# Optimization experiments

Hardware: AMD Instinct MI355X
Metric: run time of the kernel (lower is better)

The kernel has to match this reference:

```python
import jax, jax.numpy as jnp
import numpy as np

N, E, F, G, C, L = 20000, 320000, 75, 64, 10, 5
EPS = 1e-5


def setup_inputs():
    key = jax.random.key(0)
    ks = jax.random.split(key, 16)
    x = jax.random.normal(ks[0], (N, 6), jnp.float32)
    edge_index = jax.random.randint(ks[1], (2, E), 0, N, dtype=jnp.int32)
    batch = jnp.sort(jax.random.randint(ks[2], (N,), 0, G, dtype=jnp.int32))
    gcn_w = jax.random.normal(ks[3], (6, F), jnp.float32) / np.sqrt(6.0)
    gcn_b = jnp.zeros((F,), jnp.float32)
    pre_w = jax.random.normal(ks[4], (L, 2 * F, F), jnp.float32) / np.sqrt(2.0 * F)
    pre_b = jnp.zeros((L, F), jnp.float32)
    post_w = jax.random.normal(ks[5], (L, 13 * F, F), jnp.float32) / np.sqrt(13.0 * F)
    post_b = jnp.zeros((L, F), jnp.float32)
    lin_w = jax.random.normal(ks[6], (L, F, F), jnp.float32) / np.sqrt(1.0 * F)
    lin_b = jnp.zeros((L, F), jnp.float32)
    bn_g = jnp.ones((L, F), jnp.float32)
    bn_b = jnp.zeros((L, F), jnp.float32)
    w1 = jax.random.normal(ks[7], (F, 50), jnp.float32) / np.sqrt(1.0 * F)
    b1 = jnp.zeros((50,), jnp.float32)
    w2 = jax.random.normal(ks[8], (50, 25), jnp.float32) / np.sqrt(50.0)
    b2 = jnp.zeros((25,), jnp.float32)
    w3 = jax.random.normal(ks[9], (25, C), jnp.float32) / np.sqrt(25.0)
    b3 = jnp.zeros((C,), jnp.float32)
    return dict(x=x, edge_index=edge_index, batch=batch, gcn_w=gcn_w, gcn_b=gcn_b,
                pre_w=pre_w, pre_b=pre_b, post_w=post_w, post_b=post_b,
                lin_w=lin_w, lin_b=lin_b, bn_g=bn_g, bn_b=bn_b,
                w1=w1, b1=b1, w2=w2, b2=b2, w3=w3, b3=b3)


def reference(x, edge_index, batch, gcn_w, gcn_b, pre_w, pre_b, post_w, post_b,
              lin_w, lin_b, bn_g, bn_b, w1, b1, w2, b2, w3, b3):
    row, col = edge_index[0], edge_index[1]  # messages flow row (j) -> col (i)
    ones_e = jnp.ones((E,), jnp.float32)

    # ---- GCNConv(6, 75) with self-loops and symmetric normalization ----
    xw = x @ gcn_w                                   # [N, F]
    deg = jax.ops.segment_sum(ones_e, col, N) + 1.0  # in-degree + self-loop
    dinv = 1.0 / jnp.sqrt(deg)
    norm_e = (dinv[row] * dinv[col])[:, None]        # [E, 1]
    h = jax.ops.segment_sum(norm_e * xw[row], col, N) + (dinv * dinv)[:, None] * xw + gcn_b

    # ---- degree-based scalers (shared by all PNA layers) ----
    cnt = jax.ops.segment_sum(ones_e, col, N)        # in-degree per node
    avg_log = jnp.mean(jnp.log(cnt + 1.0))           # avg_deg['log'] from this graph's degree histogram
    d = jnp.maximum(cnt, 1.0)
    amp = (jnp.log(d + 1.0) / avg_log)[:, None]      # amplification
    att = (avg_log / jnp.log(d + 1.0))[:, None]      # attenuation
    cnt_c = jnp.maximum(cnt, 1.0)[:, None]
    has_nb = (cnt > 0)[:, None]

    for l in range(L):
        # pre-MLP on [x_i, x_j] per edge
        m = jnp.concatenate([h[col], h[row]], axis=-1) @ pre_w[l] + pre_b[l]  # [E, F]
        s = jax.ops.segment_sum(m, col, N)
        mean = s / cnt_c
        mean_sq = jax.ops.segment_sum(m * m, col, N) / cnt_c
        std = jnp.sqrt(jax.nn.relu(mean_sq - mean * mean) + EPS)
        mn = jnp.where(has_nb, jax.ops.segment_min(m, col, N), 0.0)
        mx = jnp.where(has_nb, jax.ops.segment_max(m, col, N), 0.0)
        agg = jnp.concatenate([mean, mn, mx, std], axis=-1)          # [N, 4F]
        scaled = jnp.concatenate([agg, agg * amp, agg * att], -1)    # [N, 12F]
        o = jnp.concatenate([h, scaled], axis=-1) @ post_w[l] + post_b[l]  # post-MLP
        o = o @ lin_w[l] + lin_b[l]                                  # final lin
        mu = o.mean(axis=0)
        var = o.var(axis=0)
        o = (o - mu) / jnp.sqrt(var + EPS) * bn_g[l] + bn_b[l]       # BatchNorm (batch stats)
        h = jax.nn.relu(o)

    # ---- global_add_pool + MLP (dropout = identity in eval) ----
    g = jax.ops.segment_sum(h, batch, G)
    g = jax.nn.relu(g @ w1 + b1)
    g = jax.nn.relu(g @ w2 + b2)
    return g @ w3 + b3  # [G, C]
```

## Files before the change

### kernel.cpp

```cpp
#include <hip/hip_runtime.h>
#include <hip/hip_bf16.h>

#define NN 20000
#define EE 320000
#define FF 75
#define GG 64
#define LL 5
#define EPS 1e-5f

#define KUV 96
#define NUV 160
#define KPOST 384
#define KLIN 96

typedef short bf16x8 __attribute__((ext_vector_type(8)));
typedef float f32x4 __attribute__((ext_vector_type(4)));

__device__ inline void gAtomicAdd(float* p, float v) { unsafeAtomicAdd(p, v); }

__device__ inline ushort f2bs(float x) {
    __hip_bfloat16 b = __float2bfloat16(x);
    return *(ushort*)&b;
}

__device__ inline float bs2f(ushort u) {
    unsigned int x = ((unsigned int)u) << 16;
    return __uint_as_float(x);
}


__global__ void count_kernel(const int* __restrict__ col, int* __restrict__ cnt, int E) {
    int e = blockIdx.x * blockDim.x + threadIdx.x;
    if (e < E) atomicAdd(&cnt[col[e]], 1);
}

__global__ void dinv_partial_kernel(const int* __restrict__ cnt, float* __restrict__ dinv,
                                    float* __restrict__ scal, int* __restrict__ bsum, int N) {
    __shared__ float red[256];
    __shared__ int redi[256];
    int tid = threadIdx.x;
    int i = blockIdx.x * 256 + tid;
    float lg = 0.f;
    int cv = 0;
    if (i < N) {
        cv = cnt[i];
        float c = (float)cv;
        dinv[i] = 1.f / sqrtf(c + 1.f);
        lg = logf(c + 1.f);
    }
    red[tid] = lg;
    redi[tid] = cv;
    __syncthreads();
    for (int s = 128; s > 0; s >>= 1) {
        if (tid < s) { red[tid] += red[tid + s]; redi[tid] += redi[tid + s]; }
        __syncthreads();
    }
    if (tid == 0) {
        gAtomicAdd(&scal[0], red[0]);
        bsum[blockIdx.x] = redi[0];
    }
}

__global__ void scanb_kernel(const int* __restrict__ bsum, int* __restrict__ bbase,
                             int* __restrict__ offs, int NB) {
    __shared__ int sh[128];
    int tid = threadIdx.x;
    int v = (tid < NB) ? bsum[tid] : 0;
    sh[tid] = v;
    __syncthreads();
    for (int d = 1; d < 128; d <<= 1) {
        int t = (tid >= d) ? sh[tid - d] : 0;
        __syncthreads();
        sh[tid] += t;
        __syncthreads();
    }
    if (tid < NB) bbase[tid] = sh[tid] - v;
    if (tid == 0) offs[NN] = EE;
}

__global__ void offs_kernel(const int* __restrict__ cnt, const int* __restrict__ bbase,
                            int* __restrict__ offs, int* __restrict__ cursor, int N) {
    __shared__ int sh[256];
    int tid = threadIdx.x;
    int i = blockIdx.x * 256 + tid;
    int v = (i < N) ? cnt[i] : 0;
    sh[tid] = v;
    __syncthreads();
    for (int d = 1; d < 256; d <<= 1) {
        int t = (tid >= d) ? sh[tid - d] : 0;
        __syncthreads();
        sh[tid] += t;
        __syncthreads();
    }
    int excl = sh[tid] - v + bbase[blockIdx.x];
    if (i < N) { offs[i] = excl; cursor[i] = excl; }
}

__global__ void fill_xs_kernel(const int* __restrict__ row, const int* __restrict__ col,
                               int* __restrict__ cursor, int* __restrict__ csr,
                               const float* __restrict__ x, const float* __restrict__ gw,
                               const float* __restrict__ dinv, ushort* __restrict__ xs) {
    int idx = blockIdx.x * 256 + threadIdx.x;
    if (idx < EE) {
        int c = col[idx];
        int pos = atomicAdd(&cursor[c], 1);
        csr[pos] = row[idx];
    } else if (idx < EE + NN * 80) {
        int j = idx - EE;
        int n = j / 80, t = j % 80;
        float v = 0.f;
        if (t < FF) {
            float acc = 0.f;
#pragma unroll
            for (int k = 0; k < 6; k++) acc += x[n * 6 + k] * gw[k * FF + t];
            v = dinv[n] * acc;
        }
        xs[j] = f2bs(v);
    }
}

__global__ __launch_bounds__(64) void gcn_kernel(
    const ushort* __restrict__ xs, const float* __restrict__ dinv,
    const int* __restrict__ offs, const int* __restrict__ csr,
    const float* __restrict__ gcn_b, const int* __restrict__ cnt,
    const float* __restrict__ scal, float* __restrict__ o2,
    float* __restrict__ amp, float* __restrict__ att, int N) {
    int i = blockIdx.x;
    int lane = threadIdx.x;
    int s0 = offs[i], s1 = offs[i + 1];
    if (lane < 40) {
        float a0 = 0.f, a1 = 0.f;
        int k = s0;
        for (; k + 3 < s1; k += 4) {
            int r0 = csr[k], r1 = csr[k + 1], r2 = csr[k + 2], r3 = csr[k + 3];
            ushort2 v0 = *(const ushort2*)(xs + (size_t)r0 * 80 + 2 * lane);
            ushort2 v1 = *(const ushort2*)(xs + (size_t)r1 * 80 + 2 * lane);
            ushort2 v2 = *(const ushort2*)(xs + (size_t)r2 * 80 + 2 * lane);
            ushort2 v3 = *(const ushort2*)(xs + (size_t)r3 * 80 + 2 * lane);
            a0 += (bs2f(v0.x) + bs2f(v1.x)) + (bs2f(v2.x) + bs2f(v3.x));
            a1 += (bs2f(v0.y) + bs2f(v1.y)) + (bs2f(v2.y) + bs2f(v3.y));
        }
        for (; k < s1; k++) {
            int r0 = csr[k];
            ushort2 v0 = *(const ushort2*)(xs + (size_t)r0 * 80 + 2 * lane);
            a0 += bs2f(v0.x);
            a1 += bs2f(v0.y);
        }
        ushort2 vs = *(const ushort2*)(xs + (size_t)i * 80 + 2 * lane);
        a0 += bs2f(vs.x);
        a1 += bs2f(vs.y);
        float di = dinv[i];
        int t0 = 2 * lane, t1 = 2 * lane + 1;
        if (t0 < FF) o2[(size_t)i * 80 + t0] = di * a0 + gcn_b[t0];
        if (t1 < FF) o2[(size_t)i * 80 + t1] = di * a1 + gcn_b[t1];
    } else if (lane == 63) {
        float al = scal[0] / (float)N;
        float d = fmaxf((float)cnt[i], 1.f);
        float lg = logf(d + 1.f);
        amp[i] = lg / al;
        att[i] = al / lg;
    }
}


#define S_UV (LL * NUV * KUV)
#define S_POST (LL * 240 * KPOST)
#define S_LIN (LL * 80 * KLIN)

__global__ void prep_bt_kernel(const float* __restrict__ pre_w, const float* __restrict__ pre_b,
                               const float* __restrict__ post_w, const float* __restrict__ lin_w,
                               ushort* __restrict__ BTuv, ushort* __restrict__ BTpost,
                               ushort* __restrict__ BTlin) {
    int idx = blockIdx.x * 256 + threadIdx.x;
    if (idx < S_UV) {
        int l = idx / (NUV * KUV);
        int r = idx % (NUV * KUV);
        int c = r / KUV, k = r % KUV;
        float v = 0.f;
        if (k < FF) {
            if (c < FF) v = pre_w[((size_t)l * 150 + k) * FF + c];
            else if (c >= 80 && c < 80 + FF) v = pre_w[((size_t)l * 150 + FF + k) * FF + (c - 80)];
        } else if (k == FF && c < FF) {
            v = pre_b[l * FF + c];
        }
        BTuv[idx] = f2bs(v);
    } else if (idx < S_UV + S_POST) {
        int j = idx - S_UV;
        int l = j / (240 * KPOST);
        int r = j % (240 * KPOST);
        int c = r / KPOST, k = r % KPOST;
        float v = 0.f;
        if (k < FF) {
            if (c < FF) v = post_w[((size_t)l * 975 + k) * FF + c];
        } else if (k < 375) {
            if (c < FF) v = post_w[((size_t)l * 975 + k) * FF + c];
            else if (c >= 80 && c < 80 + FF) v = post_w[((size_t)l * 975 + k + 300) * FF + (c - 80)];
            else if (c >= 160 && c < 160 + FF) v = post_w[((size_t)l * 975 + k + 600) * FF + (c - 160)];
        }
        BTpost[j] = f2bs(v);
    } else if (idx < S_UV + S_POST + S_LIN) {
        int j = idx - S_UV - S_POST;
        int l = j / (80 * KLIN);
        int r = j % (80 * KLIN);
        int c = r / KLIN, k = r % KLIN;
        float v = (c < FF && k < FF) ? lin_w[((size_t)l * FF + k) * FF + c] : 0.f;
        BTlin[j] = f2bs(v);
    }
}


__global__ __launch_bounds__(64) void uv_bn_kernel(
    const float* __restrict__ o2, const float* __restrict__ slots,
    const float* __restrict__ bg, const float* __restrict__ bb, int apply_bn,
    const ushort* __restrict__ BT, float* __restrict__ U, ushort* __restrict__ Vb,
    ushort* __restrict__ hagg) {
    __shared__ float ssL[160];
    int lane = threadIdx.x;
    int col16 = lane & 15, quad = lane >> 4;
    int n = blockIdx.x * 16 + col16;
    const float* orow = o2 + (size_t)n * 80;
    const ushort* bbase = BT + (size_t)col16 * KUV + quad * 8;

    if (apply_bn) {
        for (int c = lane; c < 80; c += 64) {
            if (c < FF) {
                float su = 0.f, sq = 0.f;
#pragma unroll 8
                for (int s = 0; s < 32; s++) {
                    su += slots[s * 160 + c];
                    sq += slots[s * 160 + 80 + c];
                }
                float mu = su * (1.f / (float)NN);
                float var = sq * (1.f / (float)NN) - mu * mu;
                float sc = bg[c] * rsqrtf(var + EPS);
                ssL[c] = sc;
                ssL[80 + c] = bb[c] - mu * sc;
            } else {
                ssL[c] = 0.f;
                ssL[80 + c] = 0.f;
            }
        }
        __syncthreads();
    }

    f32x4 acc[10];
#pragma unroll
    for (int i = 0; i < 10; i++) acc[i] = (f32x4){0.f, 0.f, 0.f, 0.f};

#pragma unroll
    for (int kt = 0; kt < 3; kt++) {
        int kb = kt * 32 + quad * 8;
        bf16x8 af;
        if (kb < 80) {
            float4 v0 = *(const float4*)(orow + kb);
            float4 v1 = *(const float4*)(orow + kb + 4);
            float vv[8] = {v0.x, v0.y, v0.z, v0.w, v1.x, v1.y, v1.z, v1.w};
#pragma unroll
            for (int j = 0; j < 8; j++) {
                int k = kb + j;
                float v = vv[j];
                if (apply_bn) v = fmaxf(v * ssL[k] + ssL[80 + k], 0.f);
                ushort b = (k < FF) ? f2bs(v) : (k == FF ? (ushort)0x3F80 : (ushort)0);
                af[j] = (short)b;
            }
            if (kb < FF) {
                *(bf16x8*)(hagg + (size_t)n * KPOST + kb) = af;
            }
        } else {
            af = (bf16x8){0, 0, 0, 0, 0, 0, 0, 0};
        }
#pragma unroll
        for (int nt = 0; nt < 10; nt++) {
            bf16x8 bfr = *(const bf16x8*)(bbase + nt * (16 * KUV) + kt * 32);
            acc[nt] = __builtin_amdgcn_mfma_f32_16x16x32_bf16(af, bfr, acc[nt], 0, 0, 0);
        }
    }
    int n0 = blockIdx.x * 16;
#pragma unroll
    for (int nt = 0; nt < 10; nt++) {
        int col = nt * 16 + col16;
#pragma unroll
        for (int r = 0; r < 4; r++) {
            int nn = n0 + quad * 4 + r;
            if (col < FF) U[(size_t)nn * 80 + col] = acc[nt][r];
            else if (col >= 80 && col < 80 + FF) Vb[(size_t)nn * 80 + (col - 80)] = f2bs(acc[nt][r]);
        }
    }
}


__global__ __launch_bounds__(64) void post_lin_kernel(
    const ushort* __restrict__ A, const ushort* __restrict__ BT,
    const ushort* __restrict__ BL, const float* __restrict__ amp,
    const float* __restrict__ att, float* __restrict__ o2,
    float* __restrict__ slots) {
    __shared__ __align__(16) ushort olds[16 * 104];
    int lane = threadIdx.x;
    int col16 = lane & 15, quad = lane >> 4, kseg = quad * 8;
    int n0 = blockIdx.x * 16;
    const ushort* arow = A + (size_t)(n0 + col16) * KPOST + kseg;
    const ushort* bbase = BT + (size_t)col16 * KPOST + kseg;

    f32x4 acc[15];
#pragma unroll
    for (int i = 0; i < 15; i++) acc[i] = (f32x4){0.f, 0.f, 0.f, 0.f};

#pragma unroll 4
    for (int kt = 0; kt < 12; kt++) {
        bf16x8 af = *(const bf16x8*)(arow + kt * 32);
#pragma unroll
        for (int nt = 0; nt < 15; nt++) {
            bf16x8 bfr = *(const bf16x8*)(bbase + (size_t)nt * (16 * KPOST) + kt * 32);
            acc[nt] = __builtin_amdgcn_mfma_f32_16x16x32_bf16(af, bfr, acc[nt], 0, 0, 0);
        }
    }
    float ampv[4], attv[4];
#pragma unroll
    for (int r = 0; r < 4; r++) {
        int n = n0 + quad * 4 + r;
        ampv[r] = amp[n];
        attv[r] = att[n];
    }
#pragma unroll
    for (int g = 0; g < 5; g++) {
        int col = g * 16 + col16;
#pragma unroll
        for (int r = 0; r < 4; r++) {
            float ov = acc[g][r] + ampv[r] * acc[g + 5][r] + attv[r] * acc[g + 10][r];
            olds[(quad * 4 + r) * 104 + col] = (col < FF) ? f2bs(ov) : (ushort)0;
        }
    }
    *(ushort4*)(olds + (lane >> 2) * 104 + 80 + (lane & 3) * 4) = (ushort4){0, 0, 0, 0};
    __syncthreads();

    f32x4 acc2[5];
#pragma unroll
    for (int i = 0; i < 5; i++) acc2[i] = (f32x4){0.f, 0.f, 0.f, 0.f};
    const ushort* blbase = BL + (size_t)col16 * KLIN + kseg;
#pragma unroll
    for (int kt = 0; kt < 3; kt++) {
        bf16x8 af = *(const bf16x8*)(olds + col16 * 104 + kt * 32 + kseg);
#pragma unroll
        for (int nt = 0; nt < 5; nt++) {
            bf16x8 bfr = *(const bf16x8*)(blbase + nt * (16 * KLIN) + kt * 32);
            acc2[nt] = __builtin_amdgcn_mfma_f32_16x16x32_bf16(af, bfr, acc2[nt], 0, 0, 0);
        }
    }
    float* slot = slots + (blockIdx.x & 31) * 160;
#pragma unroll
    for (int nt = 0; nt < 5; nt++) {
        int col = nt * 16 + col16;
        float s = 0.f, q = 0.f;
#pragma unroll
        for (int r = 0; r < 4; r++) {
            int n = n0 + quad * 4 + r;
            float v = acc2[nt][r];
            if (col < FF) {
                o2[(size_t)n * 80 + col] = v;
                s += v;
                q += v * v;
            }
        }
        s += __shfl_xor(s, 16); s += __shfl_xor(s, 32);
        q += __shfl_xor(q, 16); q += __shfl_xor(q, 32);
        if (lane < 16 && col < FF) {
            gAtomicAdd(&slot[col], s);
            gAtomicAdd(&slot[80 + col], q);
        }
    }
}


__global__ __launch_bounds__(64) void edge_agg_kernel(
    const float* __restrict__ U, const ushort* __restrict__ V,
    const int* __restrict__ offs, const int* __restrict__ csr,
    const int* __restrict__ cnt, ushort* __restrict__ hagg) {
    int i = blockIdx.x;
    int lane = threadIdx.x;
    int s0 = offs[i], s1 = offs[i + 1];
    if (lane < 40) {
        float2 uiv = *(const float2*)(U + (size_t)i * 80 + 2 * lane);
        float ui0 = uiv.x, ui1 = uiv.y;
        float sa0 = 0.f, sq0 = 0.f, mn0 = 1e30f, mx0 = -1e30f;
        float sa1 = 0.f, sq1 = 0.f, mn1 = 1e30f, mx1 = -1e30f;
        int k = s0;
        for (; k + 3 < s1; k += 4) {
            int r0 = csr[k], r1 = csr[k + 1], r2 = csr[k + 2], r3 = csr[k + 3];
            ushort2 v0 = *(const ushort2*)(V + (size_t)r0 * 80 + 2 * lane);
            ushort2 v1 = *(const ushort2*)(V + (size_t)r1 * 80 + 2 * lane);
            ushort2 v2 = *(const ushort2*)(V + (size_t)r2 * 80 + 2 * lane);
            ushort2 v3 = *(const ushort2*)(V + (size_t)r3 * 80 + 2 * lane);
            float a0 = ui0 + bs2f(v0.x), b0 = ui0 + bs2f(v1.x);
            float c0 = ui0 + bs2f(v2.x), d0 = ui0 + bs2f(v3.x);
            float a1 = ui1 + bs2f(v0.y), b1 = ui1 + bs2f(v1.y);
            float c1 = ui1 + bs2f(v2.y), d1 = ui1 + bs2f(v3.y);
            sa0 += (a0 + b0) + (c0 + d0);
            sq0 += (a0 * a0 + b0 * b0) + (c0 * c0 + d0 * d0);
            mn0 = fminf(mn0, fminf(fminf(a0, b0), fminf(c0, d0)));
            mx0 = fmaxf(mx0, fmaxf(fmaxf(a0, b0), fmaxf(c0, d0)));
            sa1 += (a1 + b1) + (c1 + d1);
            sq1 += (a1 * a1 + b1 * b1) + (c1 * c1 + d1 * d1);
            mn1 = fminf(mn1, fminf(fminf(a1, b1), fminf(c1, d1)));
            mx1 = fmaxf(mx1, fmaxf(fmaxf(a1, b1), fmaxf(c1, d1)));
        }
        for (; k < s1; k++) {
            int r0 = csr[k];
            ushort2 v0 = *(const ushort2*)(V + (size_t)r0 * 80 + 2 * lane);
            float a0 = ui0 + bs2f(v0.x);
            float a1 = ui1 + bs2f(v0.y);
            sa0 += a0; sq0 += a0 * a0; mn0 = fminf(mn0, a0); mx0 = fmaxf(mx0, a0);
            sa1 += a1; sq1 += a1 * a1; mn1 = fminf(mn1, a1); mx1 = fmaxf(mx1, a1);
        }
        int c = cnt[i];
        float cc = fmaxf((float)c, 1.f);
        ushort* a = hagg + (size_t)i * KPOST + FF;
        int t0 = 2 * lane, t1 = 2 * lane + 1;
        {
            float mean = sa0 / cc;
            float stdv = sqrtf(fmaxf(sq0 / cc - mean * mean, 0.f) + EPS);
            if (c == 0) { mn0 = 0.f; mx0 = 0.f; }
            if (t0 < FF) {
                a[t0] = f2bs(mean);
                a[FF + t0] = f2bs(mn0);
                a[2 * FF + t0] = f2bs(mx0);
                a[3 * FF + t0] = f2bs(stdv);
            }
        }
        {
            float mean = sa1 / cc;
            float stdv = sqrtf(fmaxf(sq1 / cc - mean * mean, 0.f) + EPS);
            if (c == 0) { mn1 = 0.f; mx1 = 0.f; }
            if (t1 < FF) {
                a[t1] = f2bs(mean);
                a[FF + t1] = f2bs(mn1);
                a[2 * FF + t1] = f2bs(mx1);
                a[3 * FF + t1] = f2bs(stdv);
            }
        }
    } else if (lane >= 48 && lane < 57) {
        hagg[(size_t)i * KPOST + 375 + (lane - 48)] = 0;
    }
}


__global__ void pool_kernel(const float* __restrict__ o2, const float* __restrict__ slots,
                            const float* __restrict__ bg, const float* __restrict__ bb,
                            const int* __restrict__ batch, float* __restrict__ g, int N) {
    __shared__ float acc[GG * FF];
    __shared__ float ssL[160];
    int tid = threadIdx.x;
    int n0 = blockIdx.x * 64;
    int n1 = min(n0 + 64, N);
    if (n0 >= N) return;
    for (int c = tid; c < 80; c += 256) {
        if (c < FF) {
            float su = 0.f, sq = 0.f;
#pragma unroll 8
            for (int s = 0; s < 32; s++) {
                su += slots[s * 160 + c];
                sq += slots[s * 160 + 80 + c];
            }
            float mu = su * (1.f / (float)NN);
            float var = sq * (1.f / (float)NN) - mu * mu;
            float sc = bg[c] * rsqrtf(var + EPS);
            ssL[c] = sc;
            ssL[80 + c] = bb[c] - mu * sc;
        } else {
            ssL[c] = 0.f;
            ssL[80 + c] = 0.f;
        }
    }
    int g0 = batch[n0];
    int g1 = batch[n1 - 1];
    int range = g1 - g0 + 1;
    for (int i = tid; i < range * FF; i += 256) acc[i] = 0.f;
    __syncthreads();
    int rows = n1 - n0;
    for (int idx = tid; idx < rows * FF; idx += 256) {
        int r = idx / FF, c = idx % FF;
        int n = n0 + r;
        float val = fmaxf(o2[(size_t)n * 80 + c] * ssL[c] + ssL[80 + c], 0.f);
        gAtomicAdd(&acc[(batch[n] - g0) * FF + c], val);
    }
    __syncthreads();
    for (int i = tid; i < range * FF; i += 256) gAtomicAdd(&g[g0 * FF + i], acc[i]);
}

__global__ void mlp_kernel(const float* __restrict__ g,
                           const float* __restrict__ w1, const float* __restrict__ b1,
                           const float* __restrict__ w2, const float* __restrict__ b2,
                           const float* __restrict__ w3, const float* __restrict__ b3,
                           float* __restrict__ out) {
    __shared__ float gr[FF], h1[50], h2[25];
    int gi = blockIdx.x, t = threadIdx.x;
    for (int j = t; j < FF; j += 64) gr[j] = g[gi * FF + j];
    __syncthreads();
    if (t < 50) {
        float a = b1[t];
        for (int k = 0; k < FF; k++) a += gr[k] * w1[k * 50 + t];
        h1[t] = fmaxf(a, 0.f);
    }
    __syncthreads();
    if (t < 25) {
        float a = b2[t];
        for (int k = 0; k < 50; k++) a += h1[k] * w2[k * 25 + t];
        h2[t] = fmaxf(a, 0.f);
    }
    __syncthreads();
    if (t < 10) {
        float a = b3[t];
        for (int k = 0; k < 25; k++) a += h2[k] * w3[k * 10 + t];
        out[gi * 10 + t] = a;
    }
}


extern "C" void kernel_launch(void* const* d_in, const int* in_sizes, int n_in,
                              void* d_out, int out_size, void* d_ws, size_t ws_size,
                              hipStream_t stream) {
    const float* x = (const float*)d_in[0];
    const int* ei = (const int*)d_in[1];
    const int* batch = (const int*)d_in[2];
    const float* gcn_w = (const float*)d_in[3];
    const float* gcn_b = (const float*)d_in[4];
    const float* pre_w = (const float*)d_in[5];
    const float* pre_b = (const float*)d_in[6];
    const float* post_w = (const float*)d_in[7];
    const float* lin_w = (const float*)d_in[9];
    const float* bn_g = (const float*)d_in[11];
    const float* bn_b = (const float*)d_in[12];
    const float* w1 = (const float*)d_in[13];
    const float* b1 = (const float*)d_in[14];
    const float* w2 = (const float*)d_in[15];
    const float* b2 = (const float*)d_in[16];
    const float* w3 = (const float*)d_in[17];
    const float* b3 = (const float*)d_in[18];
    float* out = (float*)d_out;

    const int* row = ei;
    const int* col = ei + EE;

    char* ws = (char*)d_ws;
    size_t off = 0;
    auto alloc = [&](size_t bytes) {
        char* p = ws + off;
        off += (bytes + 255) & ~(size_t)255;
        return p;
    };
    int* cnt = (int*)alloc(NN * 4);
    int* offs = (int*)alloc((NN + 1) * 4);
    int* cursor = (int*)alloc(NN * 4);
    int* csr = (int*)alloc(EE * 4);
    int* bsum = (int*)alloc(128 * 4);
    int* bbase = (int*)alloc(128 * 4);
    float* dinv = (float*)alloc(NN * 4);
    float* amp = (float*)alloc(NN * 4);
    float* att = (float*)alloc(NN * 4);
    float* scal = (float*)alloc((1 + LL * 32 * 160) * 4);
    float* slotbase = scal + 1;
    float* o2 = (float*)alloc((size_t)NN * 80 * 4);
    float* ubuf = (float*)alloc((size_t)NN * 80 * 4);
    ushort* vbuf = (ushort*)alloc((size_t)NN * 80 * 2);
    ushort* hagg = (ushort*)alloc((size_t)NN * KPOST * 2);
    ushort* BTuv = (ushort*)alloc((size_t)S_UV * 2);
    ushort* BTpost = (ushort*)alloc((size_t)S_POST * 2);
    ushort* BTlin = (ushort*)alloc((size_t)S_LIN * 2);
    float* gbuf = (float*)alloc(GG * FF * 4);

    hipMemsetAsync(cnt, 0, NN * 4, stream);
    hipMemsetAsync(scal, 0, (1 + LL * 32 * 160) * 4, stream);
    hipMemsetAsync(gbuf, 0, GG * FF * 4, stream);

    const int B = 256;
    const int NB = (NN + 255) / 256;
    count_kernel<<<(EE + B - 1) / B, B, 0, stream>>>(col, cnt, EE);
    dinv_partial_kernel<<<NB, B, 0, stream>>>(cnt, dinv, scal, bsum, NN);
    scanb_kernel<<<1, 128, 0, stream>>>(bsum, bbase, offs, NB);
    offs_kernel<<<NB, B, 0, stream>>>(cnt, bbase, offs, cursor, NN);
    fill_xs_kernel<<<(EE + NN * 80 + B - 1) / B, B, 0, stream>>>(row, col, cursor, csr,
                                                                 x, gcn_w, dinv, vbuf);
    gcn_kernel<<<NN, 64, 0, stream>>>(vbuf, dinv, offs, csr, gcn_b, cnt, scal,
                                      o2, amp, att, NN);
    {
        int tot = S_UV + S_POST + S_LIN;
        prep_bt_kernel<<<(tot + B - 1) / B, B, 0, stream>>>(pre_w, pre_b, post_w, lin_w,
                                                            BTuv, BTpost, BTlin);
    }

    const int GS = NN / 16;
    for (int l = 0; l < LL; l++) {
        float* slots_prev = slotbase + (l - 1) * 32 * 160;
        float* slots = slotbase + l * 32 * 160;
        int lp = (l > 0) ? (l - 1) : 0;
        int ab = (l > 0) ? 1 : 0;
        const float* sp = (l == 0) ? slotbase : slots_prev;

        uv_bn_kernel<<<GS, 64, 0, stream>>>(o2, sp, bn_g + lp * FF, bn_b + lp * FF, ab,
                                            BTuv + (size_t)l * NUV * KUV, ubuf, vbuf, hagg);
        edge_agg_kernel<<<NN, 64, 0, stream>>>(ubuf, vbuf, offs, csr, cnt, hagg);
        post_lin_kernel<<<GS, 64, 0, stream>>>(hagg, BTpost + (size_t)l * 240 * KPOST,
                                               BTlin + (size_t)l * 80 * KLIN, amp, att,
                                               o2, slots);
    }

    pool_kernel<<<(NN + 63) / 64, 256, 0, stream>>>(o2, slotbase + (LL - 1) * 32 * 160,
                                                    bn_g + (LL - 1) * FF, bn_b + (LL - 1) * FF,
                                                    batch, gbuf, NN);
    mlp_kernel<<<GG, 64, 0, stream>>>(gbuf, w1, b1, w2, b2, w3, b3, out);
}
```

Before: 486.8 us.

## Fuse pooling with MLP, unroll gathers by eight, merge memsets

Global add pooling and the final MLP now run in one kernel with one block per graph. Each block finds its node range by binary search over the sorted batch vector, which removes the shared-memory and global atomics and one kernel launch. The edge gather loops in the GCN and edge-aggregation kernels now load eight neighbor indices and rows per iteration instead of four, to raise memory-level parallelism. The three memsets become one contiguous memset of the counters and slot buffer. The pooling stage now has only 64 blocks, each reading about 300 rows, so its parallelism is lower.

Measured after the change: 496.5 us. Within noise of the previous version (+2.0%).

```diff
diff --git a/kernel.cpp b/kernel.cpp
--- a/kernel.cpp
+++ b/kernel.cpp
@@ -131,14 +131,16 @@
     if (lane < 40) {
         float a0 = 0.f, a1 = 0.f;
         int k = s0;
-        for (; k + 3 < s1; k += 4) {
-            int r0 = csr[k], r1 = csr[k + 1], r2 = csr[k + 2], r3 = csr[k + 3];
-            ushort2 v0 = *(const ushort2*)(xs + (size_t)r0 * 80 + 2 * lane);
-            ushort2 v1 = *(const ushort2*)(xs + (size_t)r1 * 80 + 2 * lane);
-            ushort2 v2 = *(const ushort2*)(xs + (size_t)r2 * 80 + 2 * lane);
-            ushort2 v3 = *(const ushort2*)(xs + (size_t)r3 * 80 + 2 * lane);
-            a0 += (bs2f(v0.x) + bs2f(v1.x)) + (bs2f(v2.x) + bs2f(v3.x));
-            a1 += (bs2f(v0.y) + bs2f(v1.y)) + (bs2f(v2.y) + bs2f(v3.y));
+        for (; k + 7 < s1; k += 8) {
+            int rr[8];
+#pragma unroll
+            for (int j = 0; j < 8; j++) rr[j] = csr[k + j];
+#pragma unroll
+            for (int j = 0; j < 8; j++) {
+                ushort2 v = *(const ushort2*)(xs + (size_t)rr[j] * 80 + 2 * lane);
+                a0 += bs2f(v.x);
+                a1 += bs2f(v.y);
+            }
         }
         for (; k < s1; k++) {
             int r0 = csr[k];
@@ -384,24 +386,18 @@
         float sa0 = 0.f, sq0 = 0.f, mn0 = 1e30f, mx0 = -1e30f;
         float sa1 = 0.f, sq1 = 0.f, mn1 = 1e30f, mx1 = -1e30f;
         int k = s0;
-        for (; k + 3 < s1; k += 4) {
-            int r0 = csr[k], r1 = csr[k + 1], r2 = csr[k + 2], r3 = csr[k + 3];
-            ushort2 v0 = *(const ushort2*)(V + (size_t)r0 * 80 + 2 * lane);
-            ushort2 v1 = *(const ushort2*)(V + (size_t)r1 * 80 + 2 * lane);
-            ushort2 v2 = *(const ushort2*)(V + (size_t)r2 * 80 + 2 * lane);
-            ushort2 v3 = *(const ushort2*)(V + (size_t)r3 * 80 + 2 * lane);
-            float a0 = ui0 + bs2f(v0.x), b0 = ui0 + bs2f(v1.x);
-            float c0 = ui0 + bs2f(v2.x), d0 = ui0 + bs2f(v3.x);
-            float a1 = ui1 + bs2f(v0.y), b1 = ui1 + bs2f(v1.y);
-            float c1 = ui1 + bs2f(v2.y), d1 = ui1 + bs2f(v3.y);
-            sa0 += (a0 + b0) + (c0 + d0);
-            sq0 += (a0 * a0 + b0 * b0) + (c0 * c0 + d0 * d0);
-            mn0 = fminf(mn0, fminf(fminf(a0, b0), fminf(c0, d0)));
-            mx0 = fmaxf(mx0, fmaxf(fmaxf(a0, b0), fmaxf(c0, d0)));
-            sa1 += (a1 + b1) + (c1 + d1);
-            sq1 += (a1 * a1 + b1 * b1) + (c1 * c1 + d1 * d1);
-            mn1 = fminf(mn1, fminf(fminf(a1, b1), fminf(c1, d1)));
-            mx1 = fmaxf(mx1, fmaxf(fmaxf(a1, b1), fmaxf(c1, d1)));
+        for (; k + 7 < s1; k += 8) {
+            int rr[8];
+#pragma unroll
+            for (int j = 0; j < 8; j++) rr[j] = csr[k + j];
+#pragma unroll
+            for (int j = 0; j < 8; j++) {
+                ushort2 v = *(const ushort2*)(V + (size_t)rr[j] * 80 + 2 * lane);
+                float m0 = ui0 + bs2f(v.x);
+                float m1 = ui1 + bs2f(v.y);
+                sa0 += m0; sq0 += m0 * m0; mn0 = fminf(mn0, m0); mx0 = fmaxf(mx0, m0);
+                sa1 += m1; sq1 += m1 * m1; mn1 = fminf(mn1, m1); mx1 = fmaxf(mx1, m1);
+            }
         }
         for (; k < s1; k++) {
             int r0 = csr[k];
@@ -443,16 +439,23 @@
 }
 
 
-__global__ void pool_kernel(const float* __restrict__ o2, const float* __restrict__ slots,
-                            const float* __restrict__ bg, const float* __restrict__ bb,
-                            const int* __restrict__ batch, float* __restrict__ g, int N) {
-    __shared__ float acc[GG * FF];
+__global__ __launch_bounds__(256) void pool_mlp_kernel(
+    const float* __restrict__ o2, const float* __restrict__ slots,
+    const float* __restrict__ bg, const float* __restrict__ bb,
+    const int* __restrict__ batch,
+    const float* __restrict__ w1, const float* __restrict__ b1,
+    const float* __restrict__ w2, const float* __restrict__ b2,
+    const float* __restrict__ w3, const float* __restrict__ b3,
+    float* __restrict__ out) {
     __shared__ float ssL[160];
+    __shared__ float part[240];
+    __shared__ float gr[FF], h1[50], h2[25];
+    __shared__ int sbound[2];
     int tid = threadIdx.x;
-    int n0 = blockIdx.x * 64;
-    int n1 = min(n0 + 64, N);
-    if (n0 >= N) return;
-    for (int c = tid; c < 80; c += 256) {
+    int g = blockIdx.x;
+
+    if (tid < 80) {
+        int c = tid;
         if (c < FF) {
             float su = 0.f, sq = 0.f;
 #pragma unroll 8
@@ -465,52 +468,46 @@
             float sc = bg[c] * rsqrtf(var + EPS);
             ssL[c] = sc;
             ssL[80 + c] = bb[c] - mu * sc;
-        } else {
-            ssL[c] = 0.f;
-            ssL[80 + c] = 0.f;
-        }
-    }
-    int g0 = batch[n0];
-    int g1 = batch[n1 - 1];
-    int range = g1 - g0 + 1;
-    for (int i = tid; i < range * FF; i += 256) acc[i] = 0.f;
-    __syncthreads();
-    int rows = n1 - n0;
-    for (int idx = tid; idx < rows * FF; idx += 256) {
-        int r = idx / FF, c = idx % FF;
-        int n = n0 + r;
-        float val = fmaxf(o2[(size_t)n * 80 + c] * ssL[c] + ssL[80 + c], 0.f);
-        gAtomicAdd(&acc[(batch[n] - g0) * FF + c], val);
-    }
-    __syncthreads();
-    for (int i = tid; i < range * FF; i += 256) gAtomicAdd(&g[g0 * FF + i], acc[i]);
-}
-
-__global__ void mlp_kernel(const float* __restrict__ g,
-                           const float* __restrict__ w1, const float* __restrict__ b1,
-                           const float* __restrict__ w2, const float* __restrict__ b2,
-                           const float* __restrict__ w3, const float* __restrict__ b3,
-                           float* __restrict__ out) {
-    __shared__ float gr[FF], h1[50], h2[25];
-    int gi = blockIdx.x, t = threadIdx.x;
-    for (int j = t; j < FF; j += 64) gr[j] = g[gi * FF + j];
-    __syncthreads();
-    if (t < 50) {
-        float a = b1[t];
-        for (int k = 0; k < FF; k++) a += gr[k] * w1[k * 50 + t];
-        h1[t] = fmaxf(a, 0.f);
-    }
-    __syncthreads();
-    if (t < 25) {
-        float a = b2[t];
-        for (int k = 0; k < 50; k++) a += h1[k] * w2[k * 25 + t];
-        h2[t] = fmaxf(a, 0.f);
-    }
-    __syncthreads();
-    if (t < 10) {
-        float a = b3[t];
-        for (int k = 0; k < 25; k++) a += h2[k] * w3[k * 10 + t];
-        out[gi * 10 + t] = a;
+        }
+    } else if (tid == 128) {
+        int lo = 0, hi = NN;
+        while (lo < hi) { int mid = (lo + hi) >> 1; if (batch[mid] < g) lo = mid + 1; else hi = mid; }
+        sbound[0] = lo;
+        lo = 0; hi = NN;
+        while (lo < hi) { int mid = (lo + hi) >> 1; if (batch[mid] < g + 1) lo = mid + 1; else hi = mid; }
+        sbound[1] = lo;
+    }
+    __syncthreads();
+    int s0p = sbound[0], s1p = sbound[1];
+
+    if (tid < 240) {
+        int c = tid % 80, seg = tid / 80;
+        float p = 0.f;
+        if (c < FF) {
+            for (int r = s0p + seg; r < s1p; r += 3)
+                p += fmaxf(o2[(size_t)r * 80 + c] * ssL[c] + ssL[80 + c], 0.f);
+        }
+        part[tid] = p;
+    }
+    __syncthreads();
+    if (tid < FF) gr[tid] = part[tid] + part[80 + tid] + part[160 + tid];
+    __syncthreads();
+    if (tid < 50) {
+        float a = b1[tid];
+        for (int k = 0; k < FF; k++) a += gr[k] * w1[k * 50 + tid];
+        h1[tid] = fmaxf(a, 0.f);
+    }
+    __syncthreads();
+    if (tid < 25) {
+        float a = b2[tid];
+        for (int k = 0; k < 50; k++) a += h1[k] * w2[k * 25 + tid];
+        h2[tid] = fmaxf(a, 0.f);
+    }
+    __syncthreads();
+    if (tid < 10) {
+        float a = b3[tid];
+        for (int k = 0; k < 25; k++) a += h2[k] * w3[k * 10 + tid];
+        out[g * 10 + tid] = a;
     }
 }
 
@@ -547,7 +544,11 @@
         off += (bytes + 255) & ~(size_t)255;
         return p;
     };
+    size_t z0 = off;
     int* cnt = (int*)alloc(NN * 4);
+    float* scal = (float*)alloc((1 + LL * 32 * 160) * 4);
+    size_t z1 = off;
+    float* slotbase = scal + 1;
     int* offs = (int*)alloc((NN + 1) * 4);
     int* cursor = (int*)alloc(NN * 4);
     int* csr = (int*)alloc(EE * 4);
@@ -556,8 +557,6 @@
     float* dinv = (float*)alloc(NN * 4);
     float* amp = (float*)alloc(NN * 4);
     float* att = (float*)alloc(NN * 4);
-    float* scal = (float*)alloc((1 + LL * 32 * 160) * 4);
-    float* slotbase = scal + 1;
     float* o2 = (float*)alloc((size_t)NN * 80 * 4);
     float* ubuf = (float*)alloc((size_t)NN * 80 * 4);
     ushort* vbuf = (ushort*)alloc((size_t)NN * 80 * 2);
@@ -565,11 +564,8 @@
     ushort* BTuv = (ushort*)alloc((size_t)S_UV * 2);
     ushort* BTpost = (ushort*)alloc((size_t)S_POST * 2);
     ushort* BTlin = (ushort*)alloc((size_t)S_LIN * 2);
-    float* gbuf = (float*)alloc(GG * FF * 4);
-
-    hipMemsetAsync(cnt, 0, NN * 4, stream);
-    hipMemsetAsync(scal, 0, (1 + LL * 32 * 160) * 4, stream);
-    hipMemsetAsync(gbuf, 0, GG * FF * 4, stream);
+
+    hipMemsetAsync(ws + z0, 0, z1 - z0, stream);
 
     const int B = 256;
     const int NB = (NN + 255) / 256;
@@ -603,8 +599,7 @@
                                                o2, slots);
     }
 
-    pool_kernel<<<(NN + 63) / 64, 256, 0, stream>>>(o2, slotbase + (LL - 1) * 32 * 160,
-                                                    bn_g + (LL - 1) * FF, bn_b + (LL - 1) * FF,
-                                                    batch, gbuf, NN);
-    mlp_kernel<<<GG, 64, 0, stream>>>(gbuf, w1, b1, w2, b2, w3, b3, out);
-}
+    pool_mlp_kernel<<<GG, 256, 0, stream>>>(o2, slotbase + (LL - 1) * 32 * 160,
+                                            bn_g + (LL - 1) * FF, bn_b + (LL - 1) * FF,
+                                            batch, w1, b1, w2, b2, w3, b3, out);
+}
```
